# Optimization experiments

Hardware: AMD Instinct MI355X
Metric: run time of the kernel (lower is better)

The kernel has to match this reference:

```python
import jax, jax.numpy as jnp
import numpy as np

B, NH, T, N, D = 4, 8, 2048, 512, 128
THETA = 2.0 ** 16
GAMMA = 0.995


def setup_inputs() -> dict:
    key = jax.random.key(0)
    kq, kv, ks = jax.random.split(key, 3)
    Q = jax.random.normal(kq, (B, NH, T, N), jnp.float32)
    V = jax.random.normal(kv, (B, NH, T, D), jnp.float32)
    S_prev = 0.01 * jax.random.normal(ks, (B, NH, N, D), jnp.float32)
    # get_freqs(N, theta=2**16): per-channel inverse frequencies
    freqs = jnp.asarray(1.0 / THETA ** (np.arange(N, dtype=np.float32) / N), jnp.float32)
    gamma = jnp.float32(GAMMA)
    return {"Q": Q, "V": V, "S_prev": S_prev, "freqs": freqs, "gamma": gamma}


def _rope(phases, v):
    """Rotary embedding with per-channel phases. phases broadcasts against v's
    last two dims (T, N); rotate-half formulation."""
    cos, sin = jnp.cos(phases), jnp.sin(phases)
    half = v.shape[-1] // 2
    v_rot = jnp.concatenate([-v[..., half:], v[..., :half]], axis=-1)
    return v * cos + v_rot * sin


def reference(Q, V, S_prev, freqs, gamma):
    # Q: (B,nh,T,N)  V: (B,nh,T,D)  S_prev: (B,nh,N,D)
    t_len = Q.shape[2]
    phases = jnp.arange(t_len, dtype=freqs.dtype)[:, None] * freqs[None, :]  # (T,N)
    QR = _rope(phases[None, None], Q)  # K == Q per the module's assert

    q_seq = jnp.moveaxis(QR, 2, 0)  # (T,B,nh,N)
    v_seq = jnp.moveaxis(V, 2, 0)   # (T,B,nh,D)

    def step(S, qv):
        q_t, v_t = qv
        out_t = jnp.einsum('bhn,bhnd->bhd', q_t, S)          # read before write
        S_new = (S + jnp.einsum('bhn,bhd->bhnd', q_t, v_t)) * gamma  # write + decay
        return S_new, out_t

    S_final, outs = jax.lax.scan(step, S_prev, (q_seq, v_seq))
    output = jnp.moveaxis(outs, 0, 2)  # (B,nh,T,D)
    return output, S_final
```

## Files before the change

### kernel.cpp

```cpp
#include <hip/hip_runtime.h>
#include <hip/hip_bf16.h>

typedef __attribute__((ext_vector_type(8))) short short8;
typedef __attribute__((ext_vector_type(4))) float f32x4;

#define MFMA16(a,b,c) __builtin_amdgcn_mfma_f32_16x16x32_bf16((a),(b),(c),0,0,0)

constexpr int BHn = 32;
constexpr int Tn  = 2048;
constexpr int Nn  = 512;
constexpr int Dn  = 128;
constexpr int CHn = 128;
constexpr int NCH = Tn / CHn;

static __device__ __forceinline__ unsigned short f2b(float x){
  __hip_bfloat16 h = __float2bfloat16(x);
  return *reinterpret_cast<unsigned short*>(&h);
}

__global__ __launch_bounds__(256) void rope_k(const float* __restrict__ Q,
                                              const float* __restrict__ freqs,
                                              unsigned short* __restrict__ QR){
  int gid = blockIdx.x * 256 + threadIdx.x;
  int np  = gid & 255;
  int t   = gid >> 8;
  float tf = (float)t;
  float f1 = freqs[np], f2 = freqs[np + 256];
  float s1, c1, s2, c2;
  sincosf(tf * f1, &s1, &c1);
  sincosf(tf * f2, &s2, &c2);
  size_t off = (size_t)t * Nn + np;
  for (int bh = 0; bh < BHn; ++bh){
    size_t base = (size_t)bh * Tn * Nn + off;
    float q1 = Q[base], q2 = Q[base + 256];
    QR[base]       = f2b(q1 * c1 - q2 * s1);
    QR[base + 256] = f2b(q2 * c2 + q1 * s2);
  }
}

__device__ __forceinline__ short8 ldfrag(const unsigned short* buf, int rowbase, int k0, int ld, int lane){
  int row = rowbase + (lane & 15);
  int col = (k0 + ((lane >> 4) << 3)) ^ ((row & 7) << 3);
  return *reinterpret_cast<const short8*>(buf + row * ld + col);
}
__device__ __forceinline__ short8 gfrag(const unsigned short* Qc, int rowbase, int k0, int lane){
  return *reinterpret_cast<const short8*>(
      Qc + (size_t)(rowbase + (lane & 15)) * Nn + k0 + ((lane >> 4) << 3));
}

__global__ __launch_bounds__(256) void pd_k(const unsigned short* __restrict__ QR,
                                            const float* __restrict__ gammap,
                                            unsigned short* __restrict__ Pt){
  __shared__ float gpow[129];
  const int tid = threadIdx.x, w = tid >> 6, lane = tid & 63;
  const int bh = blockIdx.x & 31, cc = blockIdx.x >> 5;
  if (tid < 129) gpow[tid] = powf(gammap[0], (float)tid);
  __syncthreads();
  const unsigned short* Qc = QR + (size_t)bh * Tn * Nn + (size_t)(cc * CHn) * Nn;

  int tiA, ntA, tiB, ntB;
  if      (w == 0){ tiA = 0; ntA = 1; tiB = 7; ntB = 8; }
  else if (w == 1){ tiA = 1; ntA = 2; tiB = 6; ntB = 7; }
  else if (w == 2){ tiA = 2; ntA = 3; tiB = 5; ntB = 6; }
  else            { tiA = 3; ntA = 4; tiB = 4; ntB = 5; }

  f32x4 accA[4], accB[8];
  #pragma unroll
  for (int t = 0; t < 4; ++t) accA[t] = {0.f, 0.f, 0.f, 0.f};
  #pragma unroll
  for (int t = 0; t < 8; ++t) accB[t] = {0.f, 0.f, 0.f, 0.f};

  for (int kb = 0; kb < 16; ++kb){
    int k0 = kb * 32;
    short8 faA = gfrag(Qc, tiA * 16, k0, lane);
    short8 faB = gfrag(Qc, tiB * 16, k0, lane);
    #pragma unroll
    for (int tj = 0; tj < 8; ++tj){
      short8 fb = gfrag(Qc, tj * 16, k0, lane);
      if (tj < ntA) accA[tj] = MFMA16(faA, fb, accA[tj]);
      if (tj < ntB) accB[tj] = MFMA16(faB, fb, accB[tj]);
    }
  }

  unsigned short* Pq = Pt + (size_t)(bh * NCH + cc) * (CHn * CHn);
  auto pw = [&](f32x4 pa, int ti, int tj, bool diag){
    int jg = tj * 16 + (lane & 15);
    int i0 = ti * 16 + ((lane >> 4) << 2);
    #pragma unroll
    for (int r = 0; r < 4; ++r){
      int ig = i0 + r;
      float v = (!diag || (jg < ig)) ? pa[r] * gpow[ig] : 0.f;
      Pq[ig * CHn + (jg ^ ((ig & 7) << 3))] = f2b(v);
    }
  };
  #pragma unroll
  for (int tj = 0; tj < 4; ++tj) if (tj < ntA) pw(accA[tj], tiA, tj, tj == ntA - 1);
  #pragma unroll
  for (int tj = 0; tj < 8; ++tj) if (tj < ntB) pw(accB[tj], tiB, tj, tj == ntB - 1);

  int zi[3], zj[3];
  if      (w == 0){ zi[0]=4; zj[0]=5; zi[1]=4; zj[1]=6; zi[2]=4; zj[2]=7; }
  else if (w == 1){ zi[0]=5; zj[0]=6; zi[1]=5; zj[1]=7; zi[2]=0; zj[2]=1; }
  else if (w == 2){ zi[0]=6; zj[0]=7; zi[1]=0; zj[1]=2; zi[2]=0; zj[2]=3; }
  else            { zi[0]=1; zj[0]=2; zi[1]=1; zj[1]=3; zi[2]=2; zj[2]=3; }
  #pragma unroll
  for (int z = 0; z < 3; ++z){
    int jg = zj[z] * 16 + (lane & 15);
    int i0 = zi[z] * 16 + ((lane >> 4) << 2);
    #pragma unroll
    for (int r = 0; r < 4; ++r){
      int ig = i0 + r;
      Pq[ig * CHn + (jg ^ ((ig & 7) << 3))] = 0;
    }
  }
}

__global__ __launch_bounds__(512, 1) void lattn_main(
    const unsigned short* __restrict__ QR,
    const unsigned short* __restrict__ Pt,
    const float* __restrict__ V,
    const float* __restrict__ S_prev,
    const float* __restrict__ gammap,
    float* __restrict__ Out,
    float* __restrict__ Sfin)
{
  __shared__ __align__(16) unsigned short SbTs[16 * 512];
  __shared__ __align__(16) unsigned short VTs[2][16 * 128];
  __shared__ float gpow[129], gpinv[129];

  const int tid  = threadIdx.x;
  const int w    = tid >> 6;
  const int lane = tid & 63;
  const int bh   = blockIdx.x & 31;
  const int dch  = blockIdx.x >> 5;
  const int d0   = dch * 16;
  const float g  = gammap[0];

  const unsigned short* QRbh = QR + (size_t)bh * Tn * Nn;
  const unsigned short* Ptbh = Pt + (size_t)bh * NCH * (CHn * CHn);
  const float* Vbh = V + (size_t)bh * Tn * Dn;

  if (tid < 129){
    gpow[tid]  = powf(g,  (float)tid);
    gpinv[tid] = powf(g, -(float)tid);
  }

  const int snt = (w < 4) ? 2 : 6;
  const int sb  = (w < 4) ? w * 2 : 8 + (w - 4) * 6;
  f32x4 st[6];
  #pragma unroll
  for (int j = 0; j < 6; ++j) if (j < snt){
    int n = (sb + j) * 16 + (lane & 15);
    st[j] = *reinterpret_cast<const f32x4*>(
        S_prev + (size_t)bh * Nn * Dn + (size_t)n * Dn + d0 + ((lane >> 4) << 2));
  }
  __syncthreads();
  const float g128 = gpow[128];

  #pragma unroll
  for (int j = 0; j < 6; ++j) if (j < snt){
    int n  = (sb + j) * 16 + (lane & 15);
    int dl = (lane >> 4) << 2;
    #pragma unroll
    for (int r = 0; r < 4; ++r){
      int d = dl + r;
      SbTs[d * 512 + (n ^ ((d & 7) << 3))] = f2b(st[j][r]);
    }
  }
  {
    int dtv = tid >> 2, dp0 = (tid & 3) << 2;
    f32x4 v4 = *reinterpret_cast<const f32x4*>(Vbh + (size_t)dtv * Dn + d0 + dp0);
    float sc = gpinv[dtv];
    #pragma unroll
    for (int r = 0; r < 4; ++r){
      int d = dp0 + r;
      VTs[0][d * 128 + (dtv ^ ((d & 7) << 3))] = f2b(v4[r] * sc);
    }
  }
  __syncthreads();

  for (int c = 0; c < NCH; ++c){
    const int t0 = c * CHn;
    const int vb = c & 1;
    const bool pf = (c + 1 < NCH);
    const unsigned short* Qc = QRbh + (size_t)t0 * Nn;

    f32x4 va4 = {0.f, 0.f, 0.f, 0.f};
    const int dtv_ = tid >> 2, dp0_ = (tid & 3) << 2;
    if (pf)
      va4 = *reinterpret_cast<const f32x4*>(Vbh + (size_t)(t0 + CHn + dtv_) * Dn + d0 + dp0_);

    if (w < 4){
      const int it0 = w, it1 = w + 4;
      f32x4 o0 = {0.f,0.f,0.f,0.f}, o1 = o0;
      for (int kb = 0; kb < 16; ++kb){
        int k0 = kb * 32;
        short8 fs = ldfrag(SbTs, 0, k0, 512, lane);
        short8 fa = gfrag(Qc, it0 * 16, k0, lane);
        short8 fb = gfrag(Qc, it1 * 16, k0, lane);
        o0 = MFMA16(fs, fa, o0);
        o1 = MFMA16(fs, fb, o1);
      }
      float g0 = gpow[it0 * 16 + (lane & 15)];
      float g1 = gpow[it1 * 16 + (lane & 15)];
      #pragma unroll
      for (int r = 0; r < 4; ++r){ o0[r] *= g0; o1[r] *= g1; }
      const unsigned short* Pq = Ptbh + (size_t)c * (CHn * CHn);
      #pragma unroll
      for (int ks = 0; ks < 4; ++ks){
        short8 av = ldfrag(VTs[vb], 0, ks * 32, 128, lane);
        if (ks < 2){
          short8 b0 = ldfrag(Pq, it0 * 16, ks * 32, CHn, lane);
          o0 = MFMA16(av, b0, o0);
        }
        short8 b1 = ldfrag(Pq, it1 * 16, ks * 32, CHn, lane);
        o1 = MFMA16(av, b1, o1);
      }
      int ti0 = t0 + it0 * 16 + (lane & 15);
      int ti1 = t0 + it1 * 16 + (lane & 15);
      *reinterpret_cast<f32x4*>(
          Out + (size_t)bh * Tn * Dn + (size_t)ti0 * Dn + d0 + ((lane >> 4) << 2)) = o0;
      *reinterpret_cast<f32x4*>(
          Out + (size_t)bh * Tn * Dn + (size_t)ti1 * Dn + d0 + ((lane >> 4) << 2)) = o1;
    }
    #pragma unroll
    for (int ks = 0; ks < 4; ++ks){
      short8 av = ldfrag(VTs[vb], 0, ks * 32, 128, lane);
      #pragma unroll
      for (int j = 0; j < 6; ++j) if (j < snt){
        int n = (sb + j) * 16 + (lane & 15);
        const unsigned short* col = Qc + (size_t)(ks * 32 + ((lane >> 4) << 3)) * Nn + n;
        short8 bn;
        #pragma unroll
        for (int e = 0; e < 8; ++e) bn[e] = (short)col[(size_t)e * Nn];
        st[j] = MFMA16(av, bn, st[j]);
      }
    }
    #pragma unroll
    for (int j = 0; j < 6; ++j) if (j < snt)
      #pragma unroll
      for (int r = 0; r < 4; ++r) st[j][r] *= g128;
    __syncthreads();

    #pragma unroll
    for (int j = 0; j < 6; ++j) if (j < snt){
      int n  = (sb + j) * 16 + (lane & 15);
      int dl = (lane >> 4) << 2;
      #pragma unroll
      for (int r = 0; r < 4; ++r){
        int d = dl + r;
        SbTs[d * 512 + (n ^ ((d & 7) << 3))] = f2b(st[j][r]);
      }
    }
    if (pf){
      float sc = gpinv[dtv_];
      #pragma unroll
      for (int r = 0; r < 4; ++r){
        int d = dp0_ + r;
        VTs[vb ^ 1][d * 128 + (dtv_ ^ ((d & 7) << 3))] = f2b(va4[r] * sc);
      }
    }
    __syncthreads();
  }

  #pragma unroll
  for (int j = 0; j < 6; ++j) if (j < snt){
    int n = (sb + j) * 16 + (lane & 15);
    *reinterpret_cast<f32x4*>(
        Sfin + (size_t)bh * Nn * Dn + (size_t)n * Dn + d0 + ((lane >> 4) << 2)) = st[j];
  }
}

extern "C" void kernel_launch(void* const* d_in, const int* in_sizes, int n_in,
                              void* d_out, int out_size, void* d_ws, size_t ws_size,
                              hipStream_t stream){
  const float* Q      = (const float*)d_in[0];
  const float* V      = (const float*)d_in[1];
  const float* S_prev = (const float*)d_in[2];
  const float* freqs  = (const float*)d_in[3];
  const float* gamma  = (const float*)d_in[4];
  float* Out  = (float*)d_out;
  float* Sfin = Out + (size_t)BHn * Tn * Dn;

  unsigned short* QR = (unsigned short*)d_ws;
  unsigned short* Pt = QR + (size_t)BHn * Tn * Nn;

  rope_k<<<2048, 256, 0, stream>>>(Q, freqs, QR);
  pd_k<<<512, 256, 0, stream>>>(QR, gamma, Pt);
  lattn_main<<<256, 512, 0, stream>>>(QR, Pt, V, S_prev, gamma, Out, Sfin);
}
```

Before: 216.9 us.

## Stage chunk Q tile in LDS for intra-chunk decay matrix kernel

The intra-chunk P-matrix kernel now loads the whole 128x512 bf16 chunk of rotated Q into swizzled shared memory once and reads MFMA fragments from LDS instead of re-reading global memory per tile. The block grows to 512 threads (8 waves), one wave per 16-row tile, and the old balanced pairing of tiles across 4 waves is replaced by a simple per-row scheme. This cuts redundant global/L2 traffic but uses 128KB of LDS per block, which limits occupancy, and leaves load imbalance across waves.

```diff
diff --git a/kernel.cpp b/kernel.cpp
--- a/kernel.cpp
+++ b/kernel.cpp
@@ -48,69 +48,50 @@
       Qc + (size_t)(rowbase + (lane & 15)) * Nn + k0 + ((lane >> 4) << 3));
 }
 
-__global__ __launch_bounds__(256) void pd_k(const unsigned short* __restrict__ QR,
-                                            const float* __restrict__ gammap,
-                                            unsigned short* __restrict__ Pt){
+__global__ __launch_bounds__(512) void pd_k2(const unsigned short* __restrict__ QR,
+                                             const float* __restrict__ gammap,
+                                             unsigned short* __restrict__ Pt){
+  __shared__ __align__(16) unsigned short Rs[128 * 512];
   __shared__ float gpow[129];
   const int tid = threadIdx.x, w = tid >> 6, lane = tid & 63;
   const int bh = blockIdx.x & 31, cc = blockIdx.x >> 5;
   if (tid < 129) gpow[tid] = powf(gammap[0], (float)tid);
+  const unsigned short* Qc = QR + (size_t)bh * Tn * Nn + (size_t)(cc * CHn) * Nn;
+  #pragma unroll
+  for (int i = 0; i < 16; ++i){
+    int p  = tid + i * 512;
+    int dt = p >> 6, n0 = (p & 63) << 3;
+    uint4 a = *reinterpret_cast<const uint4*>(Qc + (size_t)dt * Nn + n0);
+    *reinterpret_cast<uint4*>(&Rs[dt * 512 + (n0 ^ ((dt & 7) << 3))]) = a;
+  }
   __syncthreads();
-  const unsigned short* Qc = QR + (size_t)bh * Tn * Nn + (size_t)(cc * CHn) * Nn;
-
-  int tiA, ntA, tiB, ntB;
-  if      (w == 0){ tiA = 0; ntA = 1; tiB = 7; ntB = 8; }
-  else if (w == 1){ tiA = 1; ntA = 2; tiB = 6; ntB = 7; }
-  else if (w == 2){ tiA = 2; ntA = 3; tiB = 5; ntB = 6; }
-  else            { tiA = 3; ntA = 4; tiB = 4; ntB = 5; }
-
-  f32x4 accA[4], accB[8];
-  #pragma unroll
-  for (int t = 0; t < 4; ++t) accA[t] = {0.f, 0.f, 0.f, 0.f};
-  #pragma unroll
-  for (int t = 0; t < 8; ++t) accB[t] = {0.f, 0.f, 0.f, 0.f};
-
+
+  f32x4 acc[8];
+  #pragma unroll
+  for (int t = 0; t < 8; ++t) acc[t] = {0.f, 0.f, 0.f, 0.f};
   for (int kb = 0; kb < 16; ++kb){
     int k0 = kb * 32;
-    short8 faA = gfrag(Qc, tiA * 16, k0, lane);
-    short8 faB = gfrag(Qc, tiB * 16, k0, lane);
-    #pragma unroll
-    for (int tj = 0; tj < 8; ++tj){
-      short8 fb = gfrag(Qc, tj * 16, k0, lane);
-      if (tj < ntA) accA[tj] = MFMA16(faA, fb, accA[tj]);
-      if (tj < ntB) accB[tj] = MFMA16(faB, fb, accB[tj]);
+    short8 fa = ldfrag(Rs, w * 16, k0, 512, lane);
+    #pragma unroll
+    for (int tj = 0; tj < 8; ++tj) if (tj <= w){
+      short8 fb = ldfrag(Rs, tj * 16, k0, 512, lane);
+      acc[tj] = MFMA16(fa, fb, acc[tj]);
     }
   }
 
   unsigned short* Pq = Pt + (size_t)(bh * NCH + cc) * (CHn * CHn);
-  auto pw = [&](f32x4 pa, int ti, int tj, bool diag){
+  #pragma unroll
+  for (int tj = 0; tj < 8; ++tj){
     int jg = tj * 16 + (lane & 15);
-    int i0 = ti * 16 + ((lane >> 4) << 2);
+    int i0 = w * 16 + ((lane >> 4) << 2);
     #pragma unroll
     for (int r = 0; r < 4; ++r){
       int ig = i0 + r;
-      float v = (!diag || (jg < ig)) ? pa[r] * gpow[ig] : 0.f;
+      float v;
+      if (tj < w)       v = acc[tj][r] * gpow[ig];
+      else if (tj == w) v = (jg < ig) ? acc[tj][r] * gpow[ig] : 0.f;
+      else              v = 0.f;
       Pq[ig * CHn + (jg ^ ((ig & 7) << 3))] = f2b(v);
-    }
-  };
-  #pragma unroll
-  for (int tj = 0; tj < 4; ++tj) if (tj < ntA) pw(accA[tj], tiA, tj, tj == ntA - 1);
-  #pragma unroll
-  for (int tj = 0; tj < 8; ++tj) if (tj < ntB) pw(accB[tj], tiB, tj, tj == ntB - 1);
-
-  int zi[3], zj[3];
-  if      (w == 0){ zi[0]=4; zj[0]=5; zi[1]=4; zj[1]=6; zi[2]=4; zj[2]=7; }
-  else if (w == 1){ zi[0]=5; zj[0]=6; zi[1]=5; zj[1]=7; zi[2]=0; zj[2]=1; }
-  else if (w == 2){ zi[0]=6; zj[0]=7; zi[1]=0; zj[1]=2; zi[2]=0; zj[2]=3; }
-  else            { zi[0]=1; zj[0]=2; zi[1]=1; zj[1]=3; zi[2]=2; zj[2]=3; }
-  #pragma unroll
-  for (int z = 0; z < 3; ++z){
-    int jg = zj[z] * 16 + (lane & 15);
-    int i0 = zi[z] * 16 + ((lane >> 4) << 2);
-    #pragma unroll
-    for (int r = 0; r < 4; ++r){
-      int ig = i0 + r;
-      Pq[ig * CHn + (jg ^ ((ig & 7) << 3))] = 0;
     }
   }
 }
@@ -286,6 +267,6 @@
   unsigned short* Pt = QR + (size_t)BHn * Tn * Nn;
 
   rope_k<<<2048, 256, 0, stream>>>(Q, freqs, QR);
-  pd_k<<<512, 256, 0, stream>>>(QR, gamma, Pt);
+  pd_k2<<<512, 512, 0, stream>>>(QR, gamma, Pt);
   lattn_main<<<256, 512, 0, stream>>>(QR, Pt, V, S_prev, gamma, Out, Sfin);
 }
```

New measurement: 243.0 us. +12.0%, slower.

## Split sequential chunk scan into parallel update, state scan, and output kernels

Applied to the files above, without the earlier changes.

Replaces the single sequential per-(bh,dchunk) kernel with three kernels. The first computes each chunk's state increment in parallel across all chunks. A lightweight scan then accumulates the increments with decay to produce per-chunk starting states, stored in bf16 in workspace. A final fully parallel kernel computes the outputs. This removes the long serial dependency across 16 chunks that ran on only 256 blocks, at the cost of extra global traffic for the per-chunk state buffers and two more launches.

```diff
diff --git a/kernel.cpp b/kernel.cpp
--- a/kernel.cpp
+++ b/kernel.cpp
@@ -12,10 +12,17 @@
 constexpr int Dn  = 128;
 constexpr int CHn = 128;
 constexpr int NCH = Tn / CHn;
+constexpr int UDS = 16 * 512;
 
 static __device__ __forceinline__ unsigned short f2b(float x){
   __hip_bfloat16 h = __float2bfloat16(x);
   return *reinterpret_cast<unsigned short*>(&h);
+}
+static __device__ __forceinline__ float b2f(unsigned short u){
+  unsigned v = (unsigned)u << 16;
+  float f;
+  __builtin_memcpy(&f, &v, 4);
+  return f;
 }
 
 __global__ __launch_bounds__(256) void rope_k(const float* __restrict__ Q,
@@ -43,6 +50,12 @@
   int col = (k0 + ((lane >> 4) << 3)) ^ ((row & 7) << 3);
   return *reinterpret_cast<const short8*>(buf + row * ld + col);
 }
+__device__ __forceinline__ short8 ldfragT(const unsigned short* buf, int rowbase, int k0, int lane){
+  int row = rowbase + (lane & 15);
+  int sw = ((row & 7) ^ ((row >> 3) & 7)) << 3;
+  int col = (k0 + ((lane >> 4) << 3)) ^ sw;
+  return *reinterpret_cast<const short8*>(buf + row * 64 + col);
+}
 __device__ __forceinline__ short8 gfrag(const unsigned short* Qc, int rowbase, int k0, int lane){
   return *reinterpret_cast<const short8*>(
       Qc + (size_t)(rowbase + (lane & 15)) * Nn + k0 + ((lane >> 4) << 3));
@@ -115,160 +128,188 @@
   }
 }
 
-__global__ __launch_bounds__(512, 1) void lattn_main(
-    const unsigned short* __restrict__ QR,
-    const unsigned short* __restrict__ Pt,
-    const float* __restrict__ V,
-    const float* __restrict__ S_prev,
-    const float* __restrict__ gammap,
-    float* __restrict__ Out,
-    float* __restrict__ Sfin)
-{
+__global__ __launch_bounds__(512) void u_k2(const unsigned short* __restrict__ QR,
+                                            const float* __restrict__ V,
+                                            const float* __restrict__ gammap,
+                                            unsigned short* __restrict__ U){
+  __shared__ __align__(16) unsigned short RTs[512 * 64];
+  __shared__ __align__(16) unsigned short VTs[16 * 64];
+  __shared__ float gpinv[129];
+  const int tid = threadIdx.x, w = tid >> 6, lane = tid & 63;
+  const int bh = blockIdx.x & 31, cc = (blockIdx.x >> 5) & 15, dch = blockIdx.x >> 9;
+  const int d0 = dch * 16;
+  if (tid < 129) gpinv[tid] = powf(gammap[0], -(float)tid);
+  const unsigned short* Qch = QR + (size_t)bh * Tn * Nn + (size_t)(cc * CHn) * Nn;
+  const float* Vch = V + ((size_t)bh * Tn + cc * CHn) * Dn;
+  const int sb = w * 4;
+  f32x4 st[4] = {{0.f,0.f,0.f,0.f},{0.f,0.f,0.f,0.f},{0.f,0.f,0.f,0.f},{0.f,0.f,0.f,0.f}};
+
+  for (int h = 0; h < 2; ++h){
+    __syncthreads();
+    const unsigned short* Qh = Qch + (size_t)(h * 64) * Nn;
+    #pragma unroll
+    for (int i = 0; i < 4; ++i){
+      int p  = tid + i * 512;
+      int dt = (p >> 6) << 1, n0 = (p & 63) << 3;
+      const unsigned short* src = Qh + (size_t)dt * Nn + n0;
+      uint4 a = *reinterpret_cast<const uint4*>(src);
+      uint4 b = *reinterpret_cast<const uint4*>(src + Nn);
+      unsigned aw[4] = {a.x, a.y, a.z, a.w};
+      unsigned bw[4] = {b.x, b.y, b.z, b.w};
+      #pragma unroll
+      for (int e = 0; e < 8; ++e){
+        int n = n0 + e;
+        unsigned lo = (e & 1) ? (aw[e >> 1] >> 16) : (aw[e >> 1] & 0xffffu);
+        unsigned hi = (e & 1) ? (bw[e >> 1] >> 16) : (bw[e >> 1] & 0xffffu);
+        int sw = ((n & 7) ^ ((n >> 3) & 7)) << 3;
+        *reinterpret_cast<unsigned*>(&RTs[n * 64 + (dt ^ sw)]) = lo | (hi << 16);
+      }
+    }
+    {
+      int dtv = tid >> 3, dp = (tid & 7) << 1;
+      const float* vp = Vch + (size_t)(h * 64 + dtv) * Dn + d0 + dp;
+      float sc = gpinv[h * 64 + dtv];
+      VTs[ dp      * 64 + (dtv ^ (( dp      & 7) << 3))] = f2b(vp[0] * sc);
+      VTs[(dp + 1) * 64 + (dtv ^ (((dp + 1) & 7) << 3))] = f2b(vp[1] * sc);
+    }
+    __syncthreads();
+    #pragma unroll
+    for (int ks = 0; ks < 2; ++ks){
+      short8 av = ldfrag(VTs, 0, ks * 32, 64, lane);
+      #pragma unroll
+      for (int j = 0; j < 4; ++j){
+        short8 bn = ldfragT(RTs, (sb + j) * 16, ks * 32, lane);
+        st[j] = MFMA16(av, bn, st[j]);
+      }
+    }
+  }
+
+  unsigned short* Uslot = U + ((size_t)(bh * NCH + cc) * 8 + dch) * UDS;
+  #pragma unroll
+  for (int j = 0; j < 4; ++j){
+    int n  = (sb + j) * 16 + (lane & 15);
+    int dl = (lane >> 4) << 2;
+    #pragma unroll
+    for (int r = 0; r < 4; ++r){
+      int d = dl + r;
+      Uslot[d * 512 + (n ^ ((d & 7) << 3))] = f2b(st[j][r]);
+    }
+  }
+}
+
+__global__ __launch_bounds__(512) void sscan(const float* __restrict__ S_prev,
+                                             const float* __restrict__ gammap,
+                                             unsigned short* __restrict__ U,
+                                             float* __restrict__ Sfin){
+  const int tid = threadIdx.x;
+  const int bh = blockIdx.x & 31, dch = blockIdx.x >> 5;
+  const int d0 = dch * 16;
+  const float g128 = powf(gammap[0], 128.0f);
+  float st[16];
+  #pragma unroll
+  for (int e = 0; e < 16; ++e){
+    int p = tid * 16 + e;
+    int d_local = p >> 9, idx = p & 511;
+    int n = idx ^ ((d_local & 7) << 3);
+    st[e] = S_prev[((size_t)bh * Nn + n) * Dn + d0 + d_local];
+  }
+  for (int c = 0; c < NCH; ++c){
+    unsigned short* slot = U + ((size_t)(bh * NCH + c) * 8 + dch) * UDS;
+    const uint4* sp = reinterpret_cast<const uint4*>(slot + tid * 16);
+    uint4 a = sp[0], b = sp[1];
+    unsigned aw[8] = {a.x, a.y, a.z, a.w, b.x, b.y, b.z, b.w};
+    #pragma unroll
+    for (int e = 0; e < 16; ++e){
+      unsigned wb = aw[e >> 1];
+      unsigned short uv = (e & 1) ? (unsigned short)(wb >> 16) : (unsigned short)(wb & 0xffffu);
+      st[e] = (st[e] + b2f(uv)) * g128;
+    }
+    unsigned ow[8];
+    #pragma unroll
+    for (int q = 0; q < 8; ++q)
+      ow[q] = (unsigned)f2b(st[2 * q]) | ((unsigned)f2b(st[2 * q + 1]) << 16);
+    uint4* dp = reinterpret_cast<uint4*>(slot + tid * 16);
+    dp[0] = {ow[0], ow[1], ow[2], ow[3]};
+    dp[1] = {ow[4], ow[5], ow[6], ow[7]};
+  }
+  #pragma unroll
+  for (int e = 0; e < 16; ++e){
+    int p = tid * 16 + e;
+    int d_local = p >> 9, idx = p & 511;
+    int n = idx ^ ((d_local & 7) << 3);
+    Sfin[((size_t)bh * Nn + n) * Dn + d0 + d_local] = st[e];
+  }
+}
+
+__global__ __launch_bounds__(512) void out_k(const unsigned short* __restrict__ QR,
+                                             const unsigned short* __restrict__ Pt,
+                                             const unsigned short* __restrict__ U,
+                                             const float* __restrict__ V,
+                                             const float* __restrict__ S_prev,
+                                             const float* __restrict__ gammap,
+                                             float* __restrict__ Out){
   __shared__ __align__(16) unsigned short SbTs[16 * 512];
-  __shared__ __align__(16) unsigned short VTs[2][16 * 128];
+  __shared__ __align__(16) unsigned short VTs[16 * 128];
   __shared__ float gpow[129], gpinv[129];
-
-  const int tid  = threadIdx.x;
-  const int w    = tid >> 6;
-  const int lane = tid & 63;
-  const int bh   = blockIdx.x & 31;
-  const int dch  = blockIdx.x >> 5;
-  const int d0   = dch * 16;
-  const float g  = gammap[0];
-
-  const unsigned short* QRbh = QR + (size_t)bh * Tn * Nn;
-  const unsigned short* Ptbh = Pt + (size_t)bh * NCH * (CHn * CHn);
-  const float* Vbh = V + (size_t)bh * Tn * Dn;
-
+  const int tid = threadIdx.x, w = tid >> 6, lane = tid & 63;
+  const int bh = blockIdx.x & 31, dch = (blockIdx.x >> 5) & 7, cc = blockIdx.x >> 8;
+  const int d0 = dch * 16;
+  const float g = gammap[0];
   if (tid < 129){
     gpow[tid]  = powf(g,  (float)tid);
     gpinv[tid] = powf(g, -(float)tid);
   }
-
-  const int snt = (w < 4) ? 2 : 6;
-  const int sb  = (w < 4) ? w * 2 : 8 + (w - 4) * 6;
-  f32x4 st[6];
-  #pragma unroll
-  for (int j = 0; j < 6; ++j) if (j < snt){
-    int n = (sb + j) * 16 + (lane & 15);
-    st[j] = *reinterpret_cast<const f32x4*>(
-        S_prev + (size_t)bh * Nn * Dn + (size_t)n * Dn + d0 + ((lane >> 4) << 2));
+  if (cc == 0){
+    #pragma unroll
+    for (int e = 0; e < 16; ++e){
+      int p = tid * 16 + e;
+      int d_local = p >> 9, idx = p & 511;
+      int n = idx ^ ((d_local & 7) << 3);
+      SbTs[p] = f2b(S_prev[((size_t)bh * Nn + n) * Dn + d0 + d_local]);
+    }
+  } else {
+    const uint4* sp = reinterpret_cast<const uint4*>(
+        U + ((size_t)(bh * NCH + (cc - 1)) * 8 + dch) * UDS);
+    uint4* db = reinterpret_cast<uint4*>(SbTs);
+    db[tid]       = sp[tid];
+    db[tid + 512] = sp[tid + 512];
   }
   __syncthreads();
-  const float g128 = gpow[128];
-
-  #pragma unroll
-  for (int j = 0; j < 6; ++j) if (j < snt){
-    int n  = (sb + j) * 16 + (lane & 15);
-    int dl = (lane >> 4) << 2;
-    #pragma unroll
-    for (int r = 0; r < 4; ++r){
-      int d = dl + r;
-      SbTs[d * 512 + (n ^ ((d & 7) << 3))] = f2b(st[j][r]);
-    }
-  }
   {
     int dtv = tid >> 2, dp0 = (tid & 3) << 2;
-    f32x4 v4 = *reinterpret_cast<const f32x4*>(Vbh + (size_t)dtv * Dn + d0 + dp0);
+    f32x4 v4 = *reinterpret_cast<const f32x4*>(
+        V + ((size_t)bh * Tn + cc * CHn + dtv) * Dn + d0 + dp0);
     float sc = gpinv[dtv];
     #pragma unroll
     for (int r = 0; r < 4; ++r){
       int d = dp0 + r;
-      VTs[0][d * 128 + (dtv ^ ((d & 7) << 3))] = f2b(v4[r] * sc);
+      VTs[d * 128 + (dtv ^ ((d & 7) << 3))] = f2b(v4[r] * sc);
     }
   }
   __syncthreads();
 
-  for (int c = 0; c < NCH; ++c){
-    const int t0 = c * CHn;
-    const int vb = c & 1;
-    const bool pf = (c + 1 < NCH);
-    const unsigned short* Qc = QRbh + (size_t)t0 * Nn;
-
-    f32x4 va4 = {0.f, 0.f, 0.f, 0.f};
-    const int dtv_ = tid >> 2, dp0_ = (tid & 3) << 2;
-    if (pf)
-      va4 = *reinterpret_cast<const f32x4*>(Vbh + (size_t)(t0 + CHn + dtv_) * Dn + d0 + dp0_);
-
-    if (w < 4){
-      const int it0 = w, it1 = w + 4;
-      f32x4 o0 = {0.f,0.f,0.f,0.f}, o1 = o0;
-      for (int kb = 0; kb < 16; ++kb){
-        int k0 = kb * 32;
-        short8 fs = ldfrag(SbTs, 0, k0, 512, lane);
-        short8 fa = gfrag(Qc, it0 * 16, k0, lane);
-        short8 fb = gfrag(Qc, it1 * 16, k0, lane);
-        o0 = MFMA16(fs, fa, o0);
-        o1 = MFMA16(fs, fb, o1);
-      }
-      float g0 = gpow[it0 * 16 + (lane & 15)];
-      float g1 = gpow[it1 * 16 + (lane & 15)];
-      #pragma unroll
-      for (int r = 0; r < 4; ++r){ o0[r] *= g0; o1[r] *= g1; }
-      const unsigned short* Pq = Ptbh + (size_t)c * (CHn * CHn);
-      #pragma unroll
-      for (int ks = 0; ks < 4; ++ks){
-        short8 av = ldfrag(VTs[vb], 0, ks * 32, 128, lane);
-        if (ks < 2){
-          short8 b0 = ldfrag(Pq, it0 * 16, ks * 32, CHn, lane);
-          o0 = MFMA16(av, b0, o0);
-        }
-        short8 b1 = ldfrag(Pq, it1 * 16, ks * 32, CHn, lane);
-        o1 = MFMA16(av, b1, o1);
-      }
-      int ti0 = t0 + it0 * 16 + (lane & 15);
-      int ti1 = t0 + it1 * 16 + (lane & 15);
-      *reinterpret_cast<f32x4*>(
-          Out + (size_t)bh * Tn * Dn + (size_t)ti0 * Dn + d0 + ((lane >> 4) << 2)) = o0;
-      *reinterpret_cast<f32x4*>(
-          Out + (size_t)bh * Tn * Dn + (size_t)ti1 * Dn + d0 + ((lane >> 4) << 2)) = o1;
-    }
-    #pragma unroll
-    for (int ks = 0; ks < 4; ++ks){
-      short8 av = ldfrag(VTs[vb], 0, ks * 32, 128, lane);
-      #pragma unroll
-      for (int j = 0; j < 6; ++j) if (j < snt){
-        int n = (sb + j) * 16 + (lane & 15);
-        const unsigned short* col = Qc + (size_t)(ks * 32 + ((lane >> 4) << 3)) * Nn + n;
-        short8 bn;
-        #pragma unroll
-        for (int e = 0; e < 8; ++e) bn[e] = (short)col[(size_t)e * Nn];
-        st[j] = MFMA16(av, bn, st[j]);
-      }
-    }
-    #pragma unroll
-    for (int j = 0; j < 6; ++j) if (j < snt)
-      #pragma unroll
-      for (int r = 0; r < 4; ++r) st[j][r] *= g128;
-    __syncthreads();
-
-    #pragma unroll
-    for (int j = 0; j < 6; ++j) if (j < snt){
-      int n  = (sb + j) * 16 + (lane & 15);
-      int dl = (lane >> 4) << 2;
-      #pragma unroll
-      for (int r = 0; r < 4; ++r){
-        int d = dl + r;
-        SbTs[d * 512 + (n ^ ((d & 7) << 3))] = f2b(st[j][r]);
-      }
-    }
-    if (pf){
-      float sc = gpinv[dtv_];
-      #pragma unroll
-      for (int r = 0; r < 4; ++r){
-        int d = dp0_ + r;
-        VTs[vb ^ 1][d * 128 + (dtv_ ^ ((d & 7) << 3))] = f2b(va4[r] * sc);
-      }
-    }
-    __syncthreads();
-  }
-
-  #pragma unroll
-  for (int j = 0; j < 6; ++j) if (j < snt){
-    int n = (sb + j) * 16 + (lane & 15);
-    *reinterpret_cast<f32x4*>(
-        Sfin + (size_t)bh * Nn * Dn + (size_t)n * Dn + d0 + ((lane >> 4) << 2)) = st[j];
-  }
+  const unsigned short* Qc = QR + (size_t)bh * Tn * Nn + (size_t)(cc * CHn) * Nn;
+  const unsigned short* Pq = Pt + (size_t)(bh * NCH + cc) * (CHn * CHn);
+  f32x4 o = {0.f, 0.f, 0.f, 0.f};
+  for (int kb = 0; kb < 16; ++kb){
+    int k0 = kb * 32;
+    short8 fs = ldfrag(SbTs, 0, k0, 512, lane);
+    short8 fi = gfrag(Qc, w * 16, k0, lane);
+    o = MFMA16(fs, fi, o);
+  }
+  float gi = gpow[w * 16 + (lane & 15)];
+  #pragma unroll
+  for (int r = 0; r < 4; ++r) o[r] *= gi;
+  const int nks = (w >> 1) + 1;
+  #pragma unroll
+  for (int ks = 0; ks < 4; ++ks) if (ks < nks){
+    short8 av = ldfrag(VTs, 0, ks * 32, 128, lane);
+    short8 bp = ldfrag(Pq, w * 16, ks * 32, CHn, lane);
+    o = MFMA16(av, bp, o);
+  }
+  int ti = cc * CHn + w * 16 + (lane & 15);
+  *reinterpret_cast<f32x4*>(
+      Out + (size_t)bh * Tn * Dn + (size_t)ti * Dn + d0 + ((lane >> 4) << 2)) = o;
 }
 
 extern "C" void kernel_launch(void* const* d_in, const int* in_sizes, int n_in,
@@ -284,8 +325,11 @@
 
   unsigned short* QR = (unsigned short*)d_ws;
   unsigned short* Pt = QR + (size_t)BHn * Tn * Nn;
+  unsigned short* U  = Pt + (size_t)BHn * NCH * CHn * CHn;
 
   rope_k<<<2048, 256, 0, stream>>>(Q, freqs, QR);
   pd_k<<<512, 256, 0, stream>>>(QR, gamma, Pt);
-  lattn_main<<<256, 512, 0, stream>>>(QR, Pt, V, S_prev, gamma, Out, Sfin);
-}
+  u_k2<<<4096, 512, 0, stream>>>(QR, V, gamma, U);
+  sscan<<<256, 512, 0, stream>>>(S_prev, gamma, U, Sfin);
+  out_k<<<4096, 512, 0, stream>>>(QR, Pt, U, V, S_prev, gamma, Out);
+}
```

Result: slower. 292.3 us (+34.7%).
